# Kernel optimization log

Hardware: AMD Instinct MI355X
Metric: run time of the kernel (lower is better)

Reference implementation:

```python
import jax, jax.numpy as jnp
import numpy as np

# Ragged layout: 8 sequences packed into total_tokens=6144 tokens.
_SEQLENS = [1024, 512, 1024, 256, 768, 1024, 512, 1024]
_TOTAL = sum(_SEQLENS)  # 6144
_H, _D = 16, 128
_MAXLEN = 1024


def setup_inputs() -> dict:
    key = jax.random.key(0)
    kq, kk, kv = jax.random.split(key, 3)
    cu = jnp.asarray(np.concatenate([[0], np.cumsum(_SEQLENS)]), dtype=jnp.int32)
    return {
        "q": jax.random.normal(kq, (_TOTAL, _H, _D), dtype=jnp.float32),
        "k": jax.random.normal(kk, (_TOTAL, _H, _D), dtype=jnp.float32),
        "v": jax.random.normal(kv, (_TOTAL, _H, _D), dtype=jnp.float32),
        "cu_seqlens_q": cu,
        "cu_seqlens_k": cu,
        "max_seqlen_q": _MAXLEN,
        "max_seqlen_k": _MAXLEN,
    }


def _pad_gather(x, cu, L):
    """Gather packed [T,h,d] into padded [B,L,h,d] plus validity mask [B,L]."""
    starts = cu[:-1]                                   # [B]
    lens = cu[1:] - cu[:-1]                            # [B]
    pos = jnp.arange(L, dtype=cu.dtype)                # [L]
    idx = starts[:, None] + pos[None, :]               # [B,L]
    mask = pos[None, :] < lens[:, None]                # [B,L]
    idx = jnp.clip(idx, 0, x.shape[0] - 1)
    return x[idx], mask, jnp.where(mask, idx, x.shape[0])


def reference(q, k, v, cu_seqlens_q, cu_seqlens_k, max_seqlen_q, max_seqlen_k):
    # Equivalent to pytorch_varlen_attention: per-sequence SDPA (non-causal,
    # no dropout), vectorized via pad-to-max + key masking.
    T, h, d = q.shape
    qp, mq, idx_q = _pad_gather(q, cu_seqlens_q, max_seqlen_q)  # [B,Lq,h,d]
    kp, mk, _ = _pad_gather(k, cu_seqlens_k, max_seqlen_k)      # [B,Lk,h,d]
    vp, _, _ = _pad_gather(v, cu_seqlens_k, max_seqlen_k)

    scale = 1.0 / jnp.sqrt(jnp.asarray(d, dtype=q.dtype))
    scores = jnp.einsum("bqhd,bkhd->bhqk", qp, kp) * scale      # [B,h,Lq,Lk]
    neg = jnp.asarray(jnp.finfo(scores.dtype).min, scores.dtype)
    scores = jnp.where(mk[:, None, None, :], scores, neg)
    attn = jax.nn.softmax(scores, axis=-1)
    out_pad = jnp.einsum("bhqk,bkhd->bqhd", attn, vp)           # [B,Lq,h,d]

    # Scatter valid rows back to packed layout; invalid rows dropped (idx==T).
    out = jnp.zeros((T, h, d), dtype=q.dtype)
    out = out.at[idx_q.reshape(-1)].set(
        out_pad.reshape(-1, h, d), mode="drop")
    return out
```

## Files before the change

kernel.cpp:

```cpp
#include <hip/hip_runtime.h>
#include <hip/hip_bf16.h>
#include <stdint.h>

#define H 16
#define D 128
#define BM 128
#define BN 64
#define NW 4
#define NT 256

typedef __bf16 bf16_t;
typedef bf16_t bf16x8 __attribute__((ext_vector_type(8)));
typedef bf16_t bf16x2 __attribute__((ext_vector_type(2)));
typedef float f32x16 __attribute__((ext_vector_type(16)));

#define MFMA32(a, b, c) __builtin_amdgcn_mfma_f32_32x32x16_bf16(a, b, c, 0, 0, 0)

union FragU { uint32_t w[4]; bf16x8 v; };

static __device__ __forceinline__ uint32_t cvtpk_bf16(float lo, float hi) {
  uint32_t r;
  asm("v_cvt_pk_bf16_f32 %0, %1, %2" : "=v"(r) : "v"(lo), "v"(hi));
  return r;
}

static __device__ __forceinline__ void gld_lds16(const bf16_t* g, bf16_t* l) {
  __builtin_amdgcn_global_load_lds(
      (const __attribute__((address_space(1))) void*)g,
      (__attribute__((address_space(3))) void*)l, 16, 0, 0);
}


__global__ void conv_k(const float* __restrict__ kin, bf16_t* __restrict__ kb, int n8) {
  int i = blockIdx.x * blockDim.x + threadIdx.x;
  int stride = gridDim.x * blockDim.x;
  for (; i < n8; i += stride) {
    const float* p = kin + (size_t)i * 8;
    float4 a = *(const float4*)p, b = *(const float4*)(p + 4);
    bf16x8 w;
    w[0] = (bf16_t)a.x; w[1] = (bf16_t)a.y; w[2] = (bf16_t)a.z; w[3] = (bf16_t)a.w;
    w[4] = (bf16_t)b.x; w[5] = (bf16_t)b.y; w[6] = (bf16_t)b.z; w[7] = (bf16_t)b.w;
    *(bf16x8*)(kb + (size_t)i * 8) = w;
  }
}

__global__ void conv_vt(const float* __restrict__ v, bf16_t* __restrict__ vt,
                        const int* __restrict__ cuk, int nseq) {
  int tile = blockIdx.x, h = blockIdx.y;
  int acc = 0, seq = -1, lt = 0, s0k = 0, Lk = 0, Lkp = 0;
  size_t vb = 0;
  for (int s = 0; s < nseq; ++s) {
    int Ls = cuk[s + 1] - cuk[s];
    int Lp = (Ls + 63) & ~63;
    int nt = Lp / 64;
    if (tile < acc + nt) { seq = s; lt = tile - acc; s0k = cuk[s]; Lk = Ls; Lkp = Lp; break; }
    acc += nt; vb += (size_t)H * D * Lp;
  }
  if (seq < 0) return;
  int kv0 = lt * 64;
  int d = threadIdx.x;
  bf16x8 w[8];
  #pragma unroll
  for (int j = 0; j < 64; ++j) {
    int kv = kv0 + j;
    int kvc = kv < Lk ? kv : Lk - 1;
    float val = v[((size_t)(s0k + kvc) * H + h) * D + d];
    w[j >> 3][j & 7] = (bf16_t)val;
  }
  bf16_t* dstT = vt + vb + (size_t)h * D * Lkp + (size_t)lt * 8192;
  #pragma unroll
  for (int c = 0; c < 8; ++c)
    *(bf16x8*)(dstT + ((size_t)c * 128 + d) * 8) = w[c];
}


__global__ __launch_bounds__(NT, 2)
void fa_varlen6(const float* __restrict__ q,
                const bf16_t* __restrict__ kb,
                const bf16_t* __restrict__ vt,
                const int* __restrict__ cuq,
                const int* __restrict__ cuk,
                float* __restrict__ out,
                int nseq, int maxtiles)
{
  __shared__ alignas(16) bf16_t sK[2][BN * D];
  __shared__ alignas(16) bf16_t sVt[2][8 * 128 * 8];
  __shared__ float sRed[NW * 32];

  const int nwg = gridDim.x;
  const int orig = blockIdx.x;
  const int qq = nwg >> 3, rr = nwg & 7;
  const int xcd = orig & 7;
  const int wgid = (xcd < rr ? xcd * (qq + 1) : rr * (qq + 1) + (xcd - rr) * qq) + (orig >> 3);
  const int tile = wgid % maxtiles;
  const int h = wgid / maxtiles;

  int acc = 0, seq = -1, lt = 0, s0q = 0, s0k = 0, Lq = 0, Lk = 0, Lkp = 0;
  size_t vb = 0;
  for (int s = 0; s < nseq; ++s) {
    int a = cuq[s], b = cuq[s + 1];
    int Ls = b - a;
    int nt = (Ls + BM - 1) / BM;
    int Lks = cuk[s + 1] - cuk[s];
    int Lp = (Lks + 63) & ~63;
    if (tile < acc + nt) {
      seq = s; lt = tile - acc; s0q = a; Lq = Ls;
      s0k = cuk[s]; Lk = Lks; Lkp = Lp;
      break;
    }
    acc += nt; vb += (size_t)H * D * Lp;
  }
  if (seq < 0) return;

  const int q0 = lt * BM;
  const int tid = threadIdx.x;
  const int warp = tid >> 6;
  const int lane = tid & 63;
  const int lq = lane & 31;
  const int hi = lane >> 5;

  const float SC = 0.08838834764831845f * 1.44269504088896340f;

  bf16x8 qf[8];
  {
    int qrow = q0 + warp * 32 + lq; if (qrow >= Lq) qrow = Lq - 1;
    const float* qp = q + ((size_t)(s0q + qrow) * H + h) * D;
    #pragma unroll
    for (int ks = 0; ks < 8; ++ks) {
      const float* p = qp + ks * 16 + hi * 8;
      float4 a = *(const float4*)p, b = *(const float4*)(p + 4);
      bf16x8 r;
      r[0] = (bf16_t)a.x; r[1] = (bf16_t)a.y; r[2] = (bf16_t)a.z; r[3] = (bf16_t)a.w;
      r[4] = (bf16_t)b.x; r[5] = (bf16_t)b.y; r[6] = (bf16_t)b.z; r[7] = (bf16_t)b.w;
      qf[ks] = r;
    }
  }

  const bf16_t* vsrcH = vt + vb + (size_t)h * D * Lkp;

  auto STAGE = [&](int tt, int buf) {
    const int kvb = tt * BN;
    #pragma unroll
    for (int i = 0; i < 4; ++i) {
      int g = tid + i * NT;
      int row = g >> 4, cc = g & 15;
      int kvr = kvb + row; if (kvr >= Lk) kvr = Lk - 1;
      const bf16_t* src = kb + ((size_t)(s0k + kvr) * H + h) * D + ((cc ^ (row & 7)) << 3);
      gld_lds16(src, &sK[buf][g * 8]);
    }
    const bf16_t* vsrc = vsrcH + (size_t)tt * 8192;
    #pragma unroll
    for (int i = 0; i < 4; ++i) {
      int g = tid + i * NT;
      gld_lds16(vsrc + (size_t)g * 8, &sVt[buf][g * 8]);
    }
  };

  f32x16 oacc[4];
  #pragma unroll
  for (int dt = 0; dt < 4; ++dt)
    #pragma unroll
    for (int r = 0; r < 16; ++r) oacc[dt][r] = 0.f;
  float m = -1e30f, l = 0.f;

  const int nkv = (Lk + BN - 1) / BN;

  STAGE(0, 0);
  asm volatile("s_waitcnt vmcnt(0)" ::: "memory");
  __syncthreads();

  for (int t = 0; t < nkv; ++t) {
    const int cur = t & 1;
    const int kvb = t * BN;
    if (t + 1 < nkv) STAGE(t + 1, cur ^ 1);

    const bf16_t* sKc = sK[cur];
    const bf16_t* sVc = sVt[cur];
    const bool tail = (kvb + BN > Lk);

    #pragma unroll
    for (int ct = 0; ct < 2; ++ct) {
      f32x16 sa, sb;
      #pragma unroll
      for (int r = 0; r < 16; ++r) { sa[r] = 0.f; sb[r] = 0.f; }
      int krow = ct * 32 + lq;
      __builtin_amdgcn_s_setprio(1);
      #pragma unroll
      for (int ks = 0; ks < 4; ++ks) {
        int posa = (ks * 2 + hi) ^ (krow & 7);
        bf16x8 kfa = *(const bf16x8*)&sKc[krow * 128 + (posa << 3)];
        sa = MFMA32(kfa, qf[ks], sa);
        int posb = ((ks + 4) * 2 + hi) ^ (krow & 7);
        bf16x8 kfb = *(const bf16x8*)&sKc[krow * 128 + (posb << 3)];
        sb = MFMA32(kfb, qf[ks + 4], sb);
      }
      __builtin_amdgcn_s_setprio(0);

      f32x16 st;
      float tmax = -1e30f;
      #pragma unroll
      for (int r = 0; r < 16; ++r) {
        float x = (sa[r] + sb[r]) * SC;
        if (tail) {
          int kvi = kvb + ct * 32 + (r & 3) + 8 * (r >> 2) + 4 * hi;
          if (kvi >= Lk) x = -1e30f;
        }
        st[r] = x;
        tmax = fmaxf(tmax, x);
      }
      tmax = fmaxf(tmax, __shfl_xor(tmax, 32));
      bool trig = tmax > m + 8.0f;
      float mnew = trig ? tmax : m;
      float alpha = exp2f(m - mnew);
      m = mnew;

      float psum = 0.f;
      #pragma unroll
      for (int r = 0; r < 16; ++r) {
        float e = exp2f(st[r] - m);
        st[r] = e;
        psum += e;
      }
      psum += __shfl_xor(psum, 32);
      l = l * alpha + psum;

      if (__any(alpha != 1.0f)) {
        if (hi == 0) sRed[warp * 32 + lq] = alpha;
        asm volatile("s_waitcnt lgkmcnt(0)" ::: "memory");
        #pragma unroll
        for (int r = 0; r < 16; ++r) {
          float a2 = sRed[warp * 32 + (r & 3) + 8 * (r >> 2) + 4 * hi];
          #pragma unroll
          for (int dt = 0; dt < 4; ++dt) oacc[dt][r] *= a2;
        }
      }

      uint32_t c0 = cvtpk_bf16(st[0],  st[1]),  c1 = cvtpk_bf16(st[2],  st[3]);
      uint32_t c2 = cvtpk_bf16(st[4],  st[5]),  c3 = cvtpk_bf16(st[6],  st[7]);
      uint32_t c4 = cvtpk_bf16(st[8],  st[9]),  c5 = cvtpk_bf16(st[10], st[11]);
      uint32_t c6 = cvtpk_bf16(st[12], st[13]), c7 = cvtpk_bf16(st[14], st[15]);
      { auto rr2 = __builtin_amdgcn_permlane32_swap(c0, c2, false, false); c0 = rr2[0]; c2 = rr2[1]; }
      { auto rr2 = __builtin_amdgcn_permlane32_swap(c1, c3, false, false); c1 = rr2[0]; c3 = rr2[1]; }
      { auto rr2 = __builtin_amdgcn_permlane32_swap(c4, c6, false, false); c4 = rr2[0]; c6 = rr2[1]; }
      { auto rr2 = __builtin_amdgcn_permlane32_swap(c5, c7, false, false); c5 = rr2[0]; c7 = rr2[1]; }
      FragU pa, pb;
      pa.w[0] = c0; pa.w[1] = c1; pa.w[2] = c2; pa.w[3] = c3;
      pb.w[0] = c4; pb.w[1] = c5; pb.w[2] = c6; pb.w[3] = c7;

      __builtin_amdgcn_s_setprio(1);
      #pragma unroll
      for (int dt = 0; dt < 4; ++dt) {
        int drow = dt * 32 + lq;
        bf16x8 vf0 = *(const bf16x8*)&sVc[((ct * 4 + hi) * 128 + drow) << 3];
        oacc[dt] = MFMA32(pa.v, vf0, oacc[dt]);
        bf16x8 vf1 = *(const bf16x8*)&sVc[((ct * 4 + 2 + hi) * 128 + drow) << 3];
        oacc[dt] = MFMA32(pb.v, vf1, oacc[dt]);
      }
      __builtin_amdgcn_s_setprio(0);
    }

    asm volatile("s_waitcnt vmcnt(0)" ::: "memory");
    __syncthreads();
  }

  if (hi == 0) sRed[warp * 32 + lq] = l;
  asm volatile("s_waitcnt lgkmcnt(0)" ::: "memory");
  #pragma unroll
  for (int r = 0; r < 16; ++r) {
    int cr = (r & 3) + 8 * (r >> 2) + 4 * hi;
    int qr = q0 + warp * 32 + cr;
    if (qr < Lq) {
      float rn = 1.0f / sRed[warp * 32 + cr];
      float* op = out + ((size_t)(s0q + qr) * H + h) * D + lq;
      #pragma unroll
      for (int dt = 0; dt < 4; ++dt)
        op[dt * 32] = oacc[dt][r] * rn;
    }
  }
}


__global__ __launch_bounds__(NT, 3)
void fa_varlen2(const float* __restrict__ q,
                const float* __restrict__ k,
                const float* __restrict__ v,
                const int* __restrict__ cuq,
                const int* __restrict__ cuk,
                float* __restrict__ out,
                int nseq)
{
  __shared__ alignas(16) bf16_t sBuf[128 * 128];
  __shared__ float sRed[NW * 32];
  bf16_t* sK  = sBuf;
  bf16_t* sVt = sBuf + 64 * 128;

  const int tile = blockIdx.x;
  const int h = blockIdx.y;

  int acc = 0, seq = -1, lt = 0, s0q = 0, s0k = 0, Lq = 0, Lk = 0;
  for (int s = 0; s < nseq; ++s) {
    int a = cuq[s], b = cuq[s + 1];
    int Ls = b - a;
    int nt = (Ls + BM - 1) / BM;
    if (tile < acc + nt) {
      seq = s; lt = tile - acc; s0q = a; Lq = Ls;
      s0k = cuk[s]; Lk = cuk[s + 1] - s0k;
      break;
    }
    acc += nt;
  }
  if (seq < 0) return;

  const int q0 = lt * BM;
  const int tid = threadIdx.x;
  const int warp = tid >> 6;
  const int lane = tid & 63;
  const int lq = lane & 31;
  const int hi = lane >> 5;

  const float SC = 0.08838834764831845f * 1.44269504088896340f;

  #pragma unroll
  for (int ii = 0; ii < 8; ++ii) {
    int g = tid + ii * NT;
    int row = g >> 4, cc = g & 15;
    int gr = q0 + row; if (gr >= Lq) gr = Lq - 1;
    const float* p = q + ((size_t)(s0q + gr) * H + h) * D + cc * 8;
    float4 f0 = *(const float4*)p;
    float4 f1 = *(const float4*)(p + 4);
    bf16x8 w;
    w[0] = (bf16_t)f0.x; w[1] = (bf16_t)f0.y; w[2] = (bf16_t)f0.z; w[3] = (bf16_t)f0.w;
    w[4] = (bf16_t)f1.x; w[5] = (bf16_t)f1.y; w[6] = (bf16_t)f1.z; w[7] = (bf16_t)f1.w;
    *(bf16x8*)&sBuf[row * 128 + (((cc ^ (row & 7))) << 3)] = w;
  }
  __syncthreads();

  bf16x8 qf[8];
  {
    int row = warp * 32 + lq;
    #pragma unroll
    for (int ks = 0; ks < 8; ++ks) {
      int pos = (ks * 2 + hi) ^ (row & 7);
      qf[ks] = *(const bf16x8*)&sBuf[row * 128 + (pos << 3)];
    }
  }

  f32x16 oacc[4];
  #pragma unroll
  for (int dt = 0; dt < 4; ++dt)
    #pragma unroll
    for (int r = 0; r < 16; ++r) oacc[dt][r] = 0.f;
  float m = -1e30f, l = 0.f;

  const int nkv = (Lk + 63) / 64;
  for (int it = 0; it < nkv; ++it) {
    const int kv0 = it * 64;
    __syncthreads();

    #pragma unroll
    for (int ii = 0; ii < 4; ++ii) {
      int g = tid + ii * NT;
      int row = g >> 4, cc = g & 15;
      int gr = kv0 + row; if (gr >= Lk) gr = Lk - 1;
      const float* p = k + ((size_t)(s0k + gr) * H + h) * D + cc * 8;
      float4 f0 = *(const float4*)p;
      float4 f1 = *(const float4*)(p + 4);
      bf16x8 w;
      w[0] = (bf16_t)f0.x; w[1] = (bf16_t)f0.y; w[2] = (bf16_t)f0.z; w[3] = (bf16_t)f0.w;
      w[4] = (bf16_t)f1.x; w[5] = (bf16_t)f1.y; w[6] = (bf16_t)f1.z; w[7] = (bf16_t)f1.w;
      *(bf16x8*)&sK[row * 128 + (((cc ^ (row & 7))) << 3)] = w;
    }
    {
      int kp = tid & 31;
      int seg = tid >> 5;
      int r0 = kv0 + 2 * kp, r1 = r0 + 1;
      if (r0 >= Lk) r0 = Lk - 1;
      if (r1 >= Lk) r1 = Lk - 1;
      const float* p0 = v + ((size_t)(s0k + r0) * H + h) * D + seg * 16;
      const float* p1 = v + ((size_t)(s0k + r1) * H + h) * D + seg * 16;
      float va[16], vbf[16];
      *(float4*)&va[0]  = *(const float4*)p0;
      *(float4*)&va[4]  = *(const float4*)(p0 + 4);
      *(float4*)&va[8]  = *(const float4*)(p0 + 8);
      *(float4*)&va[12] = *(const float4*)(p0 + 12);
      *(float4*)&vbf[0]  = *(const float4*)p1;
      *(float4*)&vbf[4]  = *(const float4*)(p1 + 4);
      *(float4*)&vbf[8]  = *(const float4*)(p1 + 8);
      *(float4*)&vbf[12] = *(const float4*)(p1 + 12);
      int kvr = 2 * kp;
      #pragma unroll
      for (int i = 0; i < 16; ++i) {
        int d = seg * 16 + i;
        int pos = (kp >> 2) ^ (d & 7);
        bf16x2 w2; w2[0] = (bf16_t)va[i]; w2[1] = (bf16_t)vbf[i];
        *(bf16x2*)&sVt[d * 64 + (pos << 3) + (kvr & 7)] = w2;
      }
    }
    __syncthreads();

    const bool tail = (kv0 + 64 > Lk);

    #pragma unroll
    for (int ct = 0; ct < 2; ++ct) {
      f32x16 st;
      #pragma unroll
      for (int r = 0; r < 16; ++r) st[r] = 0.f;
      int krow = ct * 32 + lq;
      #pragma unroll
      for (int ks = 0; ks < 8; ++ks) {
        int pos = (ks * 2 + hi) ^ (krow & 7);
        bf16x8 kf = *(const bf16x8*)&sK[krow * 128 + (pos << 3)];
        st = MFMA32(kf, qf[ks], st);
      }

      float tmax = -1e30f;
      #pragma unroll
      for (int r = 0; r < 16; ++r) {
        float x = st[r] * SC;
        if (tail) {
          int kvi = kv0 + ct * 32 + (r & 3) + 8 * (r >> 2) + 4 * hi;
          if (kvi >= Lk) x = -1e30f;
        }
        st[r] = x;
        tmax = fmaxf(tmax, x);
      }
      tmax = fmaxf(tmax, __shfl_xor(tmax, 32));
      bool trig = tmax > m + 8.0f;
      float mnew = trig ? tmax : m;
      float alpha = exp2f(m - mnew);
      m = mnew;

      float psum = 0.f;
      #pragma unroll
      for (int r = 0; r < 16; ++r) {
        float e = exp2f(st[r] - m);
        st[r] = e;
        psum += e;
      }
      psum += __shfl_xor(psum, 32);
      l = l * alpha + psum;

      if (__any(alpha != 1.0f)) {
        if (hi == 0) sRed[warp * 32 + lq] = alpha;
        asm volatile("s_waitcnt lgkmcnt(0)" ::: "memory");
        #pragma unroll
        for (int r = 0; r < 16; ++r) {
          float a2 = sRed[warp * 32 + (r & 3) + 8 * (r >> 2) + 4 * hi];
          #pragma unroll
          for (int dt = 0; dt < 4; ++dt) oacc[dt][r] *= a2;
        }
      }

      uint32_t c0 = cvtpk_bf16(st[0],  st[1]),  c1 = cvtpk_bf16(st[2],  st[3]);
      uint32_t c2 = cvtpk_bf16(st[4],  st[5]),  c3 = cvtpk_bf16(st[6],  st[7]);
      uint32_t c4 = cvtpk_bf16(st[8],  st[9]),  c5 = cvtpk_bf16(st[10], st[11]);
      uint32_t c6 = cvtpk_bf16(st[12], st[13]), c7 = cvtpk_bf16(st[14], st[15]);
      { auto rr2 = __builtin_amdgcn_permlane32_swap(c0, c2, false, false); c0 = rr2[0]; c2 = rr2[1]; }
      { auto rr2 = __builtin_amdgcn_permlane32_swap(c1, c3, false, false); c1 = rr2[0]; c3 = rr2[1]; }
      { auto rr2 = __builtin_amdgcn_permlane32_swap(c4, c6, false, false); c4 = rr2[0]; c6 = rr2[1]; }
      { auto rr2 = __builtin_amdgcn_permlane32_swap(c5, c7, false, false); c5 = rr2[0]; c7 = rr2[1]; }
      FragU pa, pb;
      pa.w[0] = c0; pa.w[1] = c1; pa.w[2] = c2; pa.w[3] = c3;
      pb.w[0] = c4; pb.w[1] = c5; pb.w[2] = c6; pb.w[3] = c7;

      #pragma unroll
      for (int dt = 0; dt < 4; ++dt) {
        int drow = dt * 32 + lq;
        int pos0 = (ct * 4 + hi) ^ (drow & 7);
        bf16x8 vf0 = *(const bf16x8*)&sVt[drow * 64 + (pos0 << 3)];
        oacc[dt] = MFMA32(pa.v, vf0, oacc[dt]);
        int pos1 = (ct * 4 + 2 + hi) ^ (drow & 7);
        bf16x8 vf1 = *(const bf16x8*)&sVt[drow * 64 + (pos1 << 3)];
        oacc[dt] = MFMA32(pb.v, vf1, oacc[dt]);
      }
    }
  }

  if (hi == 0) sRed[warp * 32 + lq] = l;
  asm volatile("s_waitcnt lgkmcnt(0)" ::: "memory");
  #pragma unroll
  for (int r = 0; r < 16; ++r) {
    int cr = (r & 3) + 8 * (r >> 2) + 4 * hi;
    int qr = q0 + warp * 32 + cr;
    if (qr < Lq) {
      float rn = 1.0f / sRed[warp * 32 + cr];
      float* op = out + ((size_t)(s0q + qr) * H + h) * D + lq;
      #pragma unroll
      for (int dt = 0; dt < 4; ++dt)
        op[dt * 32] = oacc[dt][r] * rn;
    }
  }
}

extern "C" void kernel_launch(void* const* d_in, const int* in_sizes, int n_in,
                              void* d_out, int out_size, void* d_ws, size_t ws_size,
                              hipStream_t stream) {
  const float* q = (const float*)d_in[0];
  const float* k = (const float*)d_in[1];
  const float* v = (const float*)d_in[2];
  const int* cuq = (const int*)d_in[3];
  const int* cuk = (const int*)d_in[4];
  float* out = (float*)d_out;

  int total = in_sizes[0] / (H * D);
  int nseq = in_sizes[3] - 1;
  int maxtiles = (total + BM - 1) / BM + nseq;

  size_t needK = (size_t)in_sizes[1] * 2;
  size_t needV = (size_t)in_sizes[2] * 2 + (size_t)nseq * 64 * H * D * 2 + 256;

  if (ws_size >= needK + needV) {
    bf16_t* kb = (bf16_t*)d_ws;
    bf16_t* vtb = (bf16_t*)((char*)d_ws + needK);

    conv_k<<<1024, 256, 0, stream>>>(k, kb, in_sizes[1] / 8);
    int maxvt = (total + 63) / 64 + nseq;
    dim3 gvt(maxvt, H);
    conv_vt<<<gvt, 128, 0, stream>>>(v, vtb, cuk, nseq);
    fa_varlen6<<<dim3(maxtiles * H), NT, 0, stream>>>(q, kb, vtb, cuq, cuk, out, nseq, maxtiles);
  } else {
    dim3 grid(maxtiles, H);
    fa_varlen2<<<grid, NT, 0, stream>>>(q, k, v, cuq, cuk, out, nseq);
  }
}
```

Baseline: 130.8 us.

## Double Q tile to 256 rows with 8 warps and fold softmax scale into Q

New measurement: 202.7 us. 55.0% more time.

```diff
diff --git a/kernel.cpp b/kernel.cpp
--- a/kernel.cpp
+++ b/kernel.cpp
@@ -4,10 +4,10 @@
 
 #define H 16
 #define D 128
-#define BM 128
+#define BM 256
 #define BN 64
-#define NW 4
-#define NT 256
+#define NW 8
+#define NT 512
 
 typedef __bf16 bf16_t;
 typedef bf16_t bf16x8 __attribute__((ext_vector_type(8)));
@@ -74,8 +74,8 @@
 }
 
 
-__global__ __launch_bounds__(NT, 2)
-void fa_varlen6(const float* __restrict__ q,
+__global__ __launch_bounds__(NT, 4)
+void fa_varlen7(const float* __restrict__ q,
                 const bf16_t* __restrict__ kb,
                 const bf16_t* __restrict__ vt,
                 const int* __restrict__ cuq,
@@ -130,8 +130,10 @@
       const float* p = qp + ks * 16 + hi * 8;
       float4 a = *(const float4*)p, b = *(const float4*)(p + 4);
       bf16x8 r;
-      r[0] = (bf16_t)a.x; r[1] = (bf16_t)a.y; r[2] = (bf16_t)a.z; r[3] = (bf16_t)a.w;
-      r[4] = (bf16_t)b.x; r[5] = (bf16_t)b.y; r[6] = (bf16_t)b.z; r[7] = (bf16_t)b.w;
+      r[0] = (bf16_t)(a.x * SC); r[1] = (bf16_t)(a.y * SC);
+      r[2] = (bf16_t)(a.z * SC); r[3] = (bf16_t)(a.w * SC);
+      r[4] = (bf16_t)(b.x * SC); r[5] = (bf16_t)(b.y * SC);
+      r[6] = (bf16_t)(b.z * SC); r[7] = (bf16_t)(b.w * SC);
       qf[ks] = r;
     }
   }
@@ -141,7 +143,7 @@
   auto STAGE = [&](int tt, int buf) {
     const int kvb = tt * BN;
     #pragma unroll
-    for (int i = 0; i < 4; ++i) {
+    for (int i = 0; i < 2; ++i) {
       int g = tid + i * NT;
       int row = g >> 4, cc = g & 15;
       int kvr = kvb + row; if (kvr >= Lk) kvr = Lk - 1;
@@ -150,7 +152,7 @@
     }
     const bf16_t* vsrc = vsrcH + (size_t)tt * 8192;
     #pragma unroll
-    for (int i = 0; i < 4; ++i) {
+    for (int i = 0; i < 2; ++i) {
       int g = tid + i * NT;
       gld_lds16(vsrc + (size_t)g * 8, &sVt[buf][g * 8]);
     }
@@ -197,29 +199,42 @@
       __builtin_amdgcn_s_setprio(0);
 
       f32x16 st;
-      float tmax = -1e30f;
       #pragma unroll
       for (int r = 0; r < 16; ++r) {
-        float x = (sa[r] + sb[r]) * SC;
+        float x = sa[r] + sb[r];
         if (tail) {
           int kvi = kvb + ct * 32 + (r & 3) + 8 * (r >> 2) + 4 * hi;
           if (kvi >= Lk) x = -1e30f;
         }
         st[r] = x;
-        tmax = fmaxf(tmax, x);
-      }
-      tmax = fmaxf(tmax, __shfl_xor(tmax, 32));
-      bool trig = tmax > m + 8.0f;
-      float mnew = trig ? tmax : m;
-      float alpha = exp2f(m - mnew);
+      }
+      float m0, m1;
+      {
+        float a0 = fmaxf(st[0], st[1]),  a1 = fmaxf(st[2], st[3]);
+        float a2 = fmaxf(st[4], st[5]),  a3 = fmaxf(st[6], st[7]);
+        float a4 = fmaxf(st[8], st[9]),  a5 = fmaxf(st[10], st[11]);
+        float a6 = fmaxf(st[12], st[13]), a7 = fmaxf(st[14], st[15]);
+        float b0 = fmaxf(a0, a1), b1 = fmaxf(a2, a3);
+        float b2 = fmaxf(a4, a5), b3 = fmaxf(a6, a7);
+        m0 = fmaxf(fmaxf(b0, b1), fmaxf(b2, b3));
+      }
+      m1 = fmaxf(m0, __shfl_xor(m0, 32));
+      bool trig = m1 > m + 8.0f;
+      float mnew = trig ? m1 : m;
+      float alpha = __builtin_amdgcn_exp2f(m - mnew);
       m = mnew;
 
-      float psum = 0.f;
-      #pragma unroll
-      for (int r = 0; r < 16; ++r) {
-        float e = exp2f(st[r] - m);
-        st[r] = e;
-        psum += e;
+      #pragma unroll
+      for (int r = 0; r < 16; ++r)
+        st[r] = __builtin_amdgcn_exp2f(st[r] - m);
+      float psum;
+      {
+        float a0 = st[0] + st[1],  a1 = st[2] + st[3];
+        float a2 = st[4] + st[5],  a3 = st[6] + st[7];
+        float a4 = st[8] + st[9],  a5 = st[10] + st[11];
+        float a6 = st[12] + st[13], a7 = st[14] + st[15];
+        float b0 = a0 + a1, b1 = a2 + a3, b2 = a4 + a5, b3 = a6 + a7;
+        psum = (b0 + b1) + (b2 + b3);
       }
       psum += __shfl_xor(psum, 32);
       l = l * alpha + psum;
@@ -280,7 +295,7 @@
 }
 
 
-__global__ __launch_bounds__(NT, 3)
+__global__ __launch_bounds__(256, 3)
 void fa_varlen2(const float* __restrict__ q,
                 const float* __restrict__ k,
                 const float* __restrict__ v,
@@ -290,7 +305,7 @@
                 int nseq)
 {
   __shared__ alignas(16) bf16_t sBuf[128 * 128];
-  __shared__ float sRed[NW * 32];
+  __shared__ float sRed[4 * 32];
   bf16_t* sK  = sBuf;
   bf16_t* sVt = sBuf + 64 * 128;
 
@@ -301,7 +316,7 @@
   for (int s = 0; s < nseq; ++s) {
     int a = cuq[s], b = cuq[s + 1];
     int Ls = b - a;
-    int nt = (Ls + BM - 1) / BM;
+    int nt = (Ls + 127) / 128;
     if (tile < acc + nt) {
       seq = s; lt = tile - acc; s0q = a; Lq = Ls;
       s0k = cuk[s]; Lk = cuk[s + 1] - s0k;
@@ -311,7 +326,7 @@
   }
   if (seq < 0) return;
 
-  const int q0 = lt * BM;
+  const int q0 = lt * 128;
   const int tid = threadIdx.x;
   const int warp = tid >> 6;
   const int lane = tid & 63;
@@ -322,7 +337,7 @@
 
   #pragma unroll
   for (int ii = 0; ii < 8; ++ii) {
-    int g = tid + ii * NT;
+    int g = tid + ii * 256;
     int row = g >> 4, cc = g & 15;
     int gr = q0 + row; if (gr >= Lq) gr = Lq - 1;
     const float* p = q + ((size_t)(s0q + gr) * H + h) * D + cc * 8;
@@ -359,7 +374,7 @@
 
     #pragma unroll
     for (int ii = 0; ii < 4; ++ii) {
-      int g = tid + ii * NT;
+      int g = tid + ii * 256;
       int row = g >> 4, cc = g & 15;
       int gr = kv0 + row; if (gr >= Lk) gr = Lk - 1;
       const float* p = k + ((size_t)(s0k + gr) * H + h) * D + cc * 8;
@@ -517,9 +532,10 @@
     int maxvt = (total + 63) / 64 + nseq;
     dim3 gvt(maxvt, H);
     conv_vt<<<gvt, 128, 0, stream>>>(v, vtb, cuk, nseq);
-    fa_varlen6<<<dim3(maxtiles * H), NT, 0, stream>>>(q, kb, vtb, cuq, cuk, out, nseq, maxtiles);
+    fa_varlen7<<<dim3(maxtiles * H), NT, 0, stream>>>(q, kb, vtb, cuq, cuk, out, nseq, maxtiles);
   } else {
-    dim3 grid(maxtiles, H);
-    fa_varlen2<<<grid, NT, 0, stream>>>(q, k, v, cuq, cuk, out, nseq);
-  }
-}
+    int mt2 = (total + 127) / 128 + nseq;
+    dim3 grid(mt2, H);
+    fa_varlen2<<<grid, 256, 0, stream>>>(q, k, v, cuq, cuk, out, nseq);
+  }
+}
```
